# Optimization experiments

Measured on AMD Instinct MI355X. Metric: run time of the kernel, lower is better.

Reference implementation:

```python
import jax, jax.numpy as jnp
import numpy as np

N_NODES = 10000
DIM = 512
HEADS = 8
HEAD_DIM = DIM // HEADS  # 64
TOPK = 6
EPS = 1e-5
SLOPE = 0.01  # torch LeakyReLU default


def _layernorm(x, w, b):
    mu = x.mean(axis=-1, keepdims=True)
    var = ((x - mu) ** 2).mean(axis=-1, keepdims=True)
    return (x - mu) / jnp.sqrt(var + EPS) * w + b


def setup_inputs() -> dict:
    key = jax.random.key(0)
    ks = jax.random.split(key, 8)

    def w(k, shape):
        return jax.random.normal(k, shape, dtype=jnp.float32) * 0.02

    return {
        "x": jax.random.normal(ks[0], (1, N_NODES, DIM), dtype=jnp.float32),
        "fc1_w": w(ks[1], (DIM, DIM)), "fc1_b": jnp.zeros((DIM,), jnp.float32),
        "wh_w": w(ks[2], (DIM, DIM)), "wh_b": jnp.zeros((DIM,), jnp.float32),
        "wt_w": w(ks[3], (DIM, DIM)), "wt_b": jnp.zeros((DIM,), jnp.float32),
        "q_w": w(ks[4], (DIM, DIM)), "q_b": jnp.zeros((DIM,), jnp.float32),
        "kv_w": w(ks[5], (2 * DIM, DIM)), "kv_b": jnp.zeros((2 * DIM,), jnp.float32),
        "lin_w": w(ks[6], (DIM, DIM)), "lin_b": jnp.zeros((DIM,), jnp.float32),
        "norm_w": jnp.ones((DIM,), jnp.float32),
        "norm_b": jnp.zeros((DIM,), jnp.float32),
    }


def reference(x, fc1_w, fc1_b, wh_w, wh_b, wt_w, wt_b, q_w, q_b,
              kv_w, kv_b, lin_w, lin_b, norm_w, norm_b):
    # x: [1, N, DIM]
    n = x.shape[1]
    scale = HEAD_DIM ** -0.5

    x_input = x
    h = jax.nn.leaky_relu(x @ fc1_w.T + fc1_b, SLOPE)
    h = (h + h.mean(axis=1, keepdims=True)) * 0.5

    e_h = h @ wh_w.T + wh_b            # [1, N, DIM]
    e_t = h @ wt_w.T + wt_b            # [1, N, DIM]

    # dense graph-construction scores + per-row top-k neighbors
    logits = (e_h * scale) @ jnp.swapaxes(e_t, -2, -1)   # [1, N, N]
    _, topk_idx = jax.lax.top_k(logits, TOPK)            # [1, N, TOPK]

    # prototype node = most frequent tail index (torch unique+counts+argsort, top=1)
    counts = jnp.bincount(topk_idx.reshape(-1), length=n)
    top_node = jnp.argmax(counts)

    ins_top = jnp.take(x_input, top_node[None], axis=1)  # [1, 1, DIM]
    q_feat = jnp.take(h, top_node[None], axis=1)[0, 0]   # [DIM]

    # gather k=TOPK neighbor tail embeddings per node
    nb = e_t[0][topk_idx[0]]                              # [N, TOPK, DIM]

    q_heads = (q_feat @ q_w.T + q_b).reshape(HEADS, HEAD_DIM) * scale
    kv = (nb @ kv_w.T + kv_b).reshape(n, TOPK, 2, HEADS, HEAD_DIM)
    k_, v_ = kv[:, :, 0], kv[:, :, 1]                     # [N, TOPK, H, HD]

    attn = jnp.einsum('hd,nehd->nhe', q_heads, k_)        # [N, H, TOPK]
    attn = jax.nn.softmax(attn, axis=-1)
    out = jnp.einsum('nhe,nehd->nhd', attn, v_).reshape(n, DIM)

    e_nh = _layernorm(out, norm_w, norm_b)[None]          # [1, N, DIM]

    s = _layernorm(e_h + e_nh, norm_w, norm_b)
    s = jax.nn.leaky_relu(s @ lin_w.T + lin_b, SLOPE)     # dropout = identity (eval)
    embedding = s + x_input
    return embedding, ins_top
```

## Files before the change

### kernel.cpp

```cpp
#include <hip/hip_runtime.h>
#include <hip/hip_bf16.h>
#include <math.h>

#define N_NODES 10000
#define DIM 512
#define TOPK 6
#define NCHUNK 10
#define CHUNK 1024
#define NL 4
#define NCK 8
#define NC2 16
#define SLOPE 0.01
#define LN_EPS 1e-5f

typedef short bf16x8 __attribute__((ext_vector_type(8)));
typedef float f32x4 __attribute__((ext_vector_type(4)));
typedef double f64x4 __attribute__((ext_vector_type(4)));

__device__ __forceinline__ unsigned pack_key(float v, int idx)
{
    unsigned b = __float_as_uint(v);
    unsigned m = b ^ ((unsigned)((int)b >> 31) | 0x80000000u);
    return (m & 0xFFFFC000u) | (16383u - (unsigned)idx);
}

template <int D>
__device__ __forceinline__ void insert_u(unsigned (&k)[D], unsigned nk)
{
    if (nk > k[D - 1]) {
        k[D - 1] = nk;
#pragma unroll
        for (int s = D - 1; s > 0; s--) {
            unsigned hi = max(k[s], k[s - 1]);
            unsigned lo = min(k[s], k[s - 1]);
            k[s - 1] = hi; k[s] = lo;
        }
    }
}

template <int D>
__device__ __forceinline__ void insert_desc(float (&v)[D], int (&id)[D], float nv, int ni)
{
    if (nv > v[D - 1] || (nv == v[D - 1] && ni < id[D - 1])) {
        v[D - 1] = nv; id[D - 1] = ni;
#pragma unroll
        for (int s = D - 1; s > 0; s--) {
            bool sw = (v[s] > v[s - 1]) || (v[s] == v[s - 1] && id[s] < id[s - 1]);
            float tv = v[s]; int ti = id[s];
            if (sw) { v[s] = v[s - 1]; id[s] = id[s - 1]; v[s - 1] = tv; id[s - 1] = ti; }
        }
    }
}

__device__ __forceinline__ void gload16(const void* g, void* l)
{
    __builtin_amdgcn_global_load_lds(
        (const __attribute__((address_space(1))) void*)g,
        (__attribute__((address_space(3))) void*)l, 16, 0, 0);
}

__global__ __launch_bounds__(256) void colsum_part64(
    const double* __restrict__ h, double* __restrict__ part, int n, int nb)
{
    int b = blockIdx.x;
    int rows_per = (n + nb - 1) / nb;
    int r0 = b * rows_per, r1 = min(n, r0 + rows_per);
    int t = threadIdx.x;
    double s0 = 0.0, s1 = 0.0;
    for (int i = r0; i < r1; i++) {
        s0 += h[(size_t)i * DIM + t];
        s1 += h[(size_t)i * DIM + t + 256];
    }
    part[b * DIM + t] = s0;
    part[b * DIM + t + 256] = s1;
}

__global__ void colmean64(const double* __restrict__ part, double* __restrict__ mean,
                          int nb, int n)
{
    int j = blockIdx.x * blockDim.x + threadIdx.x;
    if (j < DIM) {
        double s = 0.0;
        for (int b = 0; b < nb; b++) s += part[b * DIM + j];
        mean[j] = s / (double)n;
    }
}

__global__ void hmix64(double* __restrict__ h, const double* __restrict__ mean, int total)
{
    int i = blockIdx.x * blockDim.x + threadIdx.x;
    if (i < total) h[i] = (h[i] + mean[i & (DIM - 1)]) * 0.5;
}

__global__ void cast_d2f_bf(const double* __restrict__ in, float* __restrict__ outf,
                            short* __restrict__ outb, int total)
{
    int i = blockIdx.x * blockDim.x + threadIdx.x;
    if (i < total) {
        float f = (float)in[i];
        outf[i] = f;
        __hip_bfloat16 b = __float2bfloat16(f);
        outb[i] = *reinterpret_cast<short*>(&b);
    }
}

__global__ void cast_f2b(const float* __restrict__ in, short* __restrict__ out, int total)
{
    int i = blockIdx.x * blockDim.x + threadIdx.x;
    if (i < total) {
        __hip_bfloat16 b = __float2bfloat16(in[i]);
        out[i] = *reinterpret_cast<short*>(&b);
    }
}

template <int POST, bool AF32>
__global__ __launch_bounds__(256, 4) void mfma_gemm_f64(
    const void* __restrict__ Av, const float* __restrict__ W,
    const float* __restrict__ bias, double* __restrict__ C,
    int n, int K, int M)
{
    __shared__ double As[64][18];
    __shared__ double Bs[64][18];
    const int t = threadIdx.x, lane = t & 63, wid = t >> 6;
    const int lx = lane & 15, q = lane >> 4;
    const int wr = (wid >> 1) * 32, wc = (wid & 1) * 32;
    const int i0 = blockIdx.x * 64, j0 = blockIdx.y * 64;

    f64x4 acc[2][2];
#pragma unroll
    for (int a = 0; a < 2; a++)
#pragma unroll
        for (int b = 0; b < 2; b++) acc[a][b] = (f64x4)0.0;

    const int srow = t >> 2, skq = (t & 3) * 4;
    int gi = i0 + srow; if (gi >= n) gi = n - 1;
    const int gj = j0 + srow;
    const float*  wrow = W + (size_t)gj * K + skq;
    const float*  af32 = (const float*)Av + (size_t)gi * K + skq;
    const double* af64 = (const double*)Av + (size_t)gi * K + skq;

    for (int k0 = 0; k0 < K; k0 += 16) {
        __syncthreads();
        if (AF32) {
            float4 v = *(const float4*)(af32 + k0);
            As[srow][skq]     = (double)v.x; As[srow][skq + 1] = (double)v.y;
            As[srow][skq + 2] = (double)v.z; As[srow][skq + 3] = (double)v.w;
        } else {
            double2 v0 = *(const double2*)(af64 + k0);
            double2 v1 = *(const double2*)(af64 + k0 + 2);
            As[srow][skq]     = v0.x; As[srow][skq + 1] = v0.y;
            As[srow][skq + 2] = v1.x; As[srow][skq + 3] = v1.y;
        }
        float4 wv = *(const float4*)(wrow + k0);
        Bs[srow][skq]     = (double)wv.x; Bs[srow][skq + 1] = (double)wv.y;
        Bs[srow][skq + 2] = (double)wv.z; Bs[srow][skq + 3] = (double)wv.w;
        __syncthreads();

#pragma unroll
        for (int ks = 0; ks < 4; ks++) {
            double a0 = As[wr + lx][ks * 4 + q];
            double a1 = As[wr + 16 + lx][ks * 4 + q];
            double b0 = Bs[wc + lx][ks * 4 + q];
            double b1 = Bs[wc + 16 + lx][ks * 4 + q];
            acc[0][0] = __builtin_amdgcn_mfma_f64_16x16x4f64(a0, b0, acc[0][0], 0, 0, 0);
            acc[0][1] = __builtin_amdgcn_mfma_f64_16x16x4f64(a0, b1, acc[0][1], 0, 0, 0);
            acc[1][0] = __builtin_amdgcn_mfma_f64_16x16x4f64(a1, b0, acc[1][0], 0, 0, 0);
            acc[1][1] = __builtin_amdgcn_mfma_f64_16x16x4f64(a1, b1, acc[1][1], 0, 0, 0);
        }
    }

#pragma unroll
    for (int rf = 0; rf < 2; rf++)
#pragma unroll
        for (int cf = 0; cf < 2; cf++)
#pragma unroll
            for (int reg = 0; reg < 4; reg++) {
                int gi2 = i0 + wr + rf * 16 + q * 4 + reg;
                int gj2 = j0 + wc + cf * 16 + lx;
                if (gi2 < n) {
                    double v = acc[rf][cf][reg] + (double)bias[gj2];
                    if (POST == 1) v = (v >= 0.0) ? v : v * SLOPE;
                    C[(size_t)gi2 * M + gj2] = v;
                }
            }
}

__global__ __launch_bounds__(256, 3) void logits_topk_mfma(
    const short* __restrict__ eh, const short* __restrict__ et,
    unsigned* __restrict__ pk, int n)
{
    __shared__ short As[2][4096];
    __shared__ short Bs[2][4096];
    const int t = threadIdx.x;
    const int lane = t & 63, wid = t >> 6;
    const int lx = lane & 15, q = lane >> 4;

    int id = blockIdx.x, bx, chunk;
    if (id < 632) { chunk = id & 7; bx = id >> 3; }
    else { int r = id - 632; chunk = 8 + (r & 1); bx = r >> 1; }
    const int i0 = bx * 128;
    const int wbase = wid * 32;

    const int jlo = chunk * CHUNK;
    const int jhi = min(n, jlo + CHUNK);
    const int nj = (jhi - jlo + 127) >> 7;
    const int np = nj * 16;

    const int sslot = (t & 3) ^ ((t >> 3) & 3);
    const short* aP[2];
    const short* bP[2];
#pragma unroll
    for (int is = 0; is < 2; is++) {
        int row = is * 64 + (t >> 2);
        int ra = i0 + row; if (ra >= n) ra = n - 1;
        aP[is] = eh + (size_t)ra * DIM + sslot * 8;
    }
    const int slotq = (q ^ ((lx >> 1) & 3)) * 8;
    const int aOff = (wbase + lx) * 32 + slotq;
    const int bOff = lx * 32 + slotq;

    unsigned keys[8][NL];
#pragma unroll
    for (int r = 0; r < 8; r++)
#pragma unroll
        for (int s = 0; s < NL; s++) keys[r][s] = 0u;

    f32x4 acc[2][8];
#pragma unroll
    for (int rf = 0; rf < 2; rf++)
#pragma unroll
        for (int cf = 0; cf < 8; cf++) acc[rf][cf] = (f32x4)0.f;

    auto STAGE = [&](int buf, int ph) {
        int kk = ph & 15;
        if (kk == 0) {
            int j0 = jlo + (ph >> 4) * 128;
#pragma unroll
            for (int is = 0; is < 2; is++) {
                int row = is * 64 + (t >> 2);
                int rb = j0 + row; if (rb >= n) rb = n - 1;
                bP[is] = et + (size_t)rb * DIM + sslot * 8;
            }
        }
        int ko = kk * 32;
#pragma unroll
        for (int is = 0; is < 2; is++) {
            gload16(aP[is] + ko, &As[buf][is * 2048 + wid * 512]);
            gload16(bP[is] + ko, &Bs[buf][is * 2048 + wid * 512]);
        }
    };

    STAGE(0, 0);
    for (int p = 0; p < np; ++p) {
        __builtin_amdgcn_sched_barrier(0);
        __builtin_amdgcn_s_barrier();
        __builtin_amdgcn_sched_barrier(0);
        if (p + 1 < np) {
            STAGE((p + 1) & 1, p + 1);
            asm volatile("s_waitcnt vmcnt(4)" ::: "memory");
        } else {
            asm volatile("s_waitcnt vmcnt(0)" ::: "memory");
        }
        __builtin_amdgcn_sched_barrier(0);
        __builtin_amdgcn_s_barrier();
        __builtin_amdgcn_sched_barrier(0);

        const short* Ab = As[p & 1];
        const short* Bb = Bs[p & 1];
        bf16x8 a0 = *(const bf16x8*)(Ab + aOff);
        bf16x8 a1 = *(const bf16x8*)(Ab + aOff + 512);
#pragma unroll
        for (int cf = 0; cf < 8; cf++) {
            bf16x8 bw = *(const bf16x8*)(Bb + bOff + cf * 512);
            acc[0][cf] = __builtin_amdgcn_mfma_f32_16x16x32_bf16(
                a0, bw, acc[0][cf], 0, 0, 0);
            acc[1][cf] = __builtin_amdgcn_mfma_f32_16x16x32_bf16(
                a1, bw, acc[1][cf], 0, 0, 0);
        }

        if ((p & 15) == 15) {
            int j0 = jlo + (p >> 4) * 128;
#pragma unroll
            for (int rf = 0; rf < 2; rf++)
#pragma unroll
                for (int cf = 0; cf < 8; cf++) {
                    int gj = j0 + cf * 16 + lx;
                    if (gj < n) {
#pragma unroll
                        for (int reg = 0; reg < 4; reg++)
                            insert_u<NL>(keys[rf * 4 + reg],
                                         pack_key(acc[rf][cf][reg], gj));
                    }
                    acc[rf][cf] = (f32x4)0.f;
                }
        }
    }

#pragma unroll
    for (int rr = 0; rr < 8; rr++) {
        unsigned mk[NCK];
#pragma unroll
        for (int s = 0; s < NL; s++) mk[s] = keys[rr][s];
#pragma unroll
        for (int s = NL; s < NCK; s++) mk[s] = 0u;
        for (int m = 1; m < 16; m <<= 1) {
            unsigned sv[NCK];
#pragma unroll
            for (int s = 0; s < NCK; s++) sv[s] = mk[s];
#pragma unroll
            for (int s = 0; s < NCK; s++) {
                unsigned ov = (unsigned)__shfl_xor((int)sv[s], m);
                insert_u<NCK>(mk, ov);
            }
        }
        if (lx == 0) {
            int rf = rr >> 2, reg = rr & 3;
            int grow = i0 + wbase + rf * 16 + q * 4 + reg;
            if (grow < n) {
#pragma unroll
                for (int s = 0; s < NCK; s++)
                    pk[((size_t)chunk * N_NODES + grow) * NCK + s] = mk[s];
            }
        }
    }
}

template <int POST>
__global__ __launch_bounds__(256, 3) void mfma_gemm_bf16(
    const short* __restrict__ A, const short* __restrict__ W,
    const float* __restrict__ bias, const float* __restrict__ res,
    float* __restrict__ C, int n, int M)
{
    __shared__ short As[2][8192];
    __shared__ short Bs[2][8192];
    const int t = threadIdx.x;
    const int lane = t & 63, wid = t >> 6;
    const int lx = lane & 15, q = lane >> 4;
    const int lx7 = lane & 7;
    const int i0 = blockIdx.x * 128;
    const int j0 = blockIdx.y * 128;
    const int wbase = wid * 32;
    const int srl = lane >> 3;
    const int swz = (lane & 7) ^ srl;

    const short* aP[4];
    const short* bP[4];
#pragma unroll
    for (int is = 0; is < 4; is++) {
        int ra = i0 + is * 32 + wid * 8 + srl; if (ra >= n) ra = n - 1;
        aP[is] = A + (size_t)ra * DIM + swz * 8;
        int rb = j0 + is * 32 + wid * 8 + srl;
        bP[is] = W + (size_t)rb * DIM + swz * 8;
    }
    int aIdx[2], bIdx[2];
#pragma unroll
    for (int ks = 0; ks < 2; ks++) {
        int kap = (ks * 4 + q) ^ lx7;
        aIdx[ks] = (wbase + lx) * 64 + kap * 8;
        bIdx[ks] = lx * 64 + kap * 8;
    }

    f32x4 acc[2][8];
#pragma unroll
    for (int rf = 0; rf < 2; rf++)
#pragma unroll
        for (int cf = 0; cf < 8; cf++) acc[rf][cf] = (f32x4)0.f;

    auto STAGE = [&](int buf, int kk) {
        int ko = kk * 64;
        short* ab = &As[buf][wid * 512];
        short* bb = &Bs[buf][wid * 512];
#pragma unroll
        for (int is = 0; is < 4; is++) {
            gload16(aP[is] + ko, ab + is * 2048);
            gload16(bP[is] + ko, bb + is * 2048);
        }
    };

    STAGE(0, 0);
    for (int p = 0; p < 8; ++p) {
        __builtin_amdgcn_sched_barrier(0);
        __builtin_amdgcn_s_barrier();
        __builtin_amdgcn_sched_barrier(0);
        if (p + 1 < 8) {
            STAGE((p + 1) & 1, p + 1);
            asm volatile("s_waitcnt vmcnt(8)" ::: "memory");
        } else {
            asm volatile("s_waitcnt vmcnt(0)" ::: "memory");
        }
        __builtin_amdgcn_sched_barrier(0);
        __builtin_amdgcn_s_barrier();
        __builtin_amdgcn_sched_barrier(0);

        const short* Ab = As[p & 1];
        const short* Bb = Bs[p & 1];
#pragma unroll
        for (int ks = 0; ks < 2; ks++) {
            bf16x8 a0 = *(const bf16x8*)(Ab + aIdx[ks]);
            bf16x8 a1 = *(const bf16x8*)(Ab + aIdx[ks] + 1024);
#pragma unroll
            for (int cf = 0; cf < 8; cf++) {
                bf16x8 bw = *(const bf16x8*)(Bb + bIdx[ks] + cf * 1024);
                acc[0][cf] = __builtin_amdgcn_mfma_f32_16x16x32_bf16(
                    a0, bw, acc[0][cf], 0, 0, 0);
                acc[1][cf] = __builtin_amdgcn_mfma_f32_16x16x32_bf16(
                    a1, bw, acc[1][cf], 0, 0, 0);
            }
        }
    }

#pragma unroll
    for (int rf = 0; rf < 2; rf++)
#pragma unroll
        for (int cf = 0; cf < 8; cf++)
#pragma unroll
            for (int reg = 0; reg < 4; reg++) {
                int gi = i0 + wbase + rf * 16 + q * 4 + reg;
                int gj = j0 + cf * 16 + lx;
                if (gi < n) {
                    float v = acc[rf][cf][reg] + bias[gj];
                    if (POST >= 1) v = (v >= 0.f) ? v : v * SLOPE;
                    if (POST == 2) v += res[(size_t)gi * M + gj];
                    C[(size_t)gi * M + gj] = v;
                }
            }
}

__global__ void merge_chunks16(const unsigned* __restrict__ pk,
                               int* __restrict__ cand, int n)
{
    int row = blockIdx.x * blockDim.x + threadIdx.x;
    if (row >= n) return;
    unsigned bk[NC2];
#pragma unroll
    for (int s = 0; s < NC2; s++) bk[s] = 0u;
    for (int c = 0; c < NCHUNK; c++) {
#pragma unroll
        for (int s = 0; s < NCK; s++)
            insert_u<NC2>(bk, pk[((size_t)c * n + row) * NCK + s]);
    }
#pragma unroll
    for (int s = 0; s < NC2; s++)
        cand[row * NC2 + s] = 16383 - (int)(bk[s] & 16383u);
}

__global__ __launch_bounds__(64) void refine16(
    const double* __restrict__ ehd, const double* __restrict__ etd,
    const int* __restrict__ cand, int* __restrict__ tki, int n)
{
    int row = blockIdx.x;
    int lane = threadIdx.x;
    int c = lane >> 2, sub = lane & 3;
    int j = cand[row * NC2 + c];
    const double* er = ehd + (size_t)row * DIM;
    const double* tr = etd + (size_t)j * DIM;
    double s = 0.0;
#pragma unroll 8
    for (int k = sub; k < DIM; k += 4) s += er[k] * tr[k];
    s += __shfl_down(s, 2);
    s += __shfl_down(s, 1);
    double mine = __shfl(s, lane & ~3);
    int rank = 0;
#pragma unroll
    for (int m = 0; m < NC2; m++) {
        double vm = __shfl(s, m * 4);
        int jm = __shfl(j, m * 4);
        bool better = (vm > mine) || (vm == mine && jm < j);
        rank += better ? 1 : 0;
    }
    if (sub == 0 && rank < TOPK) tki[row * TOPK + rank] = j;
}

__global__ void count_kernel(const int* __restrict__ tki, int* __restrict__ counts, int total)
{
    int i = blockIdx.x * blockDim.x + threadIdx.x;
    if (i < total) atomicAdd(&counts[tki[i]], 1);
}

__global__ __launch_bounds__(1024) void argmax_kernel(
    const int* __restrict__ counts, int n, const float* __restrict__ x,
    int* __restrict__ topn, float* __restrict__ out_ins)
{
    __shared__ unsigned long long red[1024];
    int t = threadIdx.x;
    unsigned long long best = 0;
    for (int j = t; j < n; j += 1024) {
        unsigned long long key =
            ((unsigned long long)(unsigned)counts[j] << 32) | (unsigned)(n - 1 - j);
        if (key > best) best = key;
    }
    red[t] = best;
    __syncthreads();
    for (int s = 512; s > 0; s >>= 1) {
        if (t < s && red[t + s] > red[t]) red[t] = red[t + s];
        __syncthreads();
    }
    int tn = n - 1 - (int)(red[0] & 0xffffffffu);
    if (t == 0) *topn = tn;
    if (t < DIM) out_ins[t] = x[(size_t)tn * DIM + t];
}

__global__ __launch_bounds__(512) void qheads_kernel(
    const double* __restrict__ h2d, const int* __restrict__ topn,
    const float* __restrict__ qw, const float* __restrict__ qb, float* __restrict__ qh)
{
    __shared__ float qf[DIM];
    int t = threadIdx.x;
    int tn = *topn;
    qf[t] = (float)h2d[(size_t)tn * DIM + t];
    __syncthreads();
    int w = t >> 6, lane = t & 63;
    int jrow = blockIdx.x * 8 + w;
    float s = 0.f;
    for (int k = lane; k < DIM; k += 64) s += qf[k] * qw[(size_t)jrow * DIM + k];
#pragma unroll
    for (int m = 32; m > 0; m >>= 1) s += __shfl_down(s, m);
    if (lane == 0) qh[jrow] = (s + qb[jrow]) * 0.125f;
}

__global__ __launch_bounds__(512) void scores_kernel(
    const float* __restrict__ E, const float* __restrict__ qh, float* __restrict__ sc)
{
    int i = blockIdx.x;
    int t = threadIdx.x, w = t >> 6, lane = t & 63;
    float v = qh[t] * E[(size_t)i * 1024 + t];
#pragma unroll
    for (int m = 32; m > 0; m >>= 1) v += __shfl_down(v, m);
    if (lane == 0) sc[i * 8 + w] = v;
}

__global__ __launch_bounds__(512) void attn_ln_kernel(
    const float* __restrict__ E, const float* __restrict__ sc,
    const int* __restrict__ tki, const float* __restrict__ eh,
    const float* __restrict__ nw, const float* __restrict__ nbias,
    short* __restrict__ sprb, int n)
{
    __shared__ int nb[TOPK];
    __shared__ float red[16];
    __shared__ float stats[2];
    const int i = blockIdx.x;
    const int t = threadIdx.x;
    const int h = t >> 6, lane = t & 63;
    if (t < TOPK) nb[t] = tki[i * TOPK + t];
    __syncthreads();

    float myse = 0.f;
    if (lane < TOPK) myse = sc[(size_t)nb[lane] * 8 + h];
    float se[TOPK];
#pragma unroll
    for (int e = 0; e < TOPK; e++) se[e] = __shfl(myse, e);
    float mx = se[0];
#pragma unroll
    for (int e = 1; e < TOPK; e++) mx = fmaxf(mx, se[e]);
    float wsum = 0.f, w[TOPK];
#pragma unroll
    for (int e = 0; e < TOPK; e++) { w[e] = expf(se[e] - mx); wsum += w[e]; }
    float inv = 1.f / wsum;

    float o = 0.f;
#pragma unroll
    for (int e = 0; e < TOPK; e++) o += w[e] * E[(size_t)nb[e] * 1024 + 512 + t];
    o *= inv;

    float s1 = o, s2 = o * o;
#pragma unroll
    for (int m = 32; m > 0; m >>= 1) { s1 += __shfl_down(s1, m); s2 += __shfl_down(s2, m); }
    if (lane == 0) { red[h] = s1; red[h + 8] = s2; }
    __syncthreads();
    if (t == 0) {
        float a = 0.f, b = 0.f;
#pragma unroll
        for (int k = 0; k < 8; k++) { a += red[k]; b += red[k + 8]; }
        float mu = a * (1.f / 512.f);
        float var = b * (1.f / 512.f) - mu * mu;
        stats[0] = mu; stats[1] = rsqrtf(var + LN_EPS);
    }
    __syncthreads();
    float enh = (o - stats[0]) * stats[1] * nw[t] + nbias[t];
    float t2 = eh[(size_t)i * DIM + t] + enh;
    __syncthreads();

    s1 = t2; s2 = t2 * t2;
#pragma unroll
    for (int m = 32; m > 0; m >>= 1) { s1 += __shfl_down(s1, m); s2 += __shfl_down(s2, m); }
    if (lane == 0) { red[h] = s1; red[h + 8] = s2; }
    __syncthreads();
    if (t == 0) {
        float a = 0.f, b = 0.f;
#pragma unroll
        for (int k = 0; k < 8; k++) { a += red[k]; b += red[k + 8]; }
        float mu = a * (1.f / 512.f);
        float var = b * (1.f / 512.f) - mu * mu;
        stats[0] = mu; stats[1] = rsqrtf(var + LN_EPS);
    }
    __syncthreads();
    float sv = (t2 - stats[0]) * stats[1] * nw[t] + nbias[t];
    __hip_bfloat16 bb = __float2bfloat16(sv);
    sprb[(size_t)i * DIM + t] = *reinterpret_cast<short*>(&bb);
}

extern "C" void kernel_launch(void* const* d_in, const int* in_sizes, int n_in,
                              void* d_out, int out_size, void* d_ws, size_t ws_size,
                              hipStream_t stream)
{
    const float* x     = (const float*)d_in[0];
    const float* fc1_w = (const float*)d_in[1];
    const float* fc1_b = (const float*)d_in[2];
    const float* wh_w  = (const float*)d_in[3];
    const float* wh_b  = (const float*)d_in[4];
    const float* wt_w  = (const float*)d_in[5];
    const float* wt_b  = (const float*)d_in[6];
    const float* q_w   = (const float*)d_in[7];
    const float* q_b   = (const float*)d_in[8];
    const float* kv_w  = (const float*)d_in[9];
    const float* kv_b  = (const float*)d_in[10];
    const float* lin_w = (const float*)d_in[11];
    const float* lin_b = (const float*)d_in[12];
    const float* nw    = (const float*)d_in[13];
    const float* nbias = (const float*)d_in[14];
    float* out = (float*)d_out;

    const int n = N_NODES;
    size_t off = 0;
    auto take = [&](size_t bytes) -> void* {
        void* p = (void*)((char*)d_ws + off);
        off += (bytes + 255) & ~(size_t)255;
        return p;
    };
    double* h2d  = (double*)take((size_t)n * DIM * 8);
    double* ehd  = (double*)take((size_t)n * DIM * 8);
    double* etd  = (double*)take((size_t)n * DIM * 8);
    float*  ehf  = (float*)take((size_t)n * DIM * 4);
    float*  etf  = (float*)take((size_t)n * DIM * 4);
    short*  ehb  = (short*)take((size_t)n * DIM * 2);
    short*  etb  = (short*)take((size_t)n * DIM * 2);
    unsigned* pk = (unsigned*)take((size_t)NCHUNK * n * NCK * 4);
    int*    cand = (int*)take((size_t)n * NC2 * 4);
    int*    tki  = (int*)take((size_t)n * TOPK * 4);
    int*    counts = (int*)take((size_t)n * 4);
    int*    topn = (int*)take(256);
    float*  qh   = (float*)take(DIM * 4);
    float*  sc   = (float*)take((size_t)n * 8 * 4);
    double* part = (double*)take((size_t)160 * DIM * 8);
    double* mean = (double*)take(DIM * 8);
    short*  kvwb = (short*)take((size_t)1024 * DIM * 2);
    short*  linwb = (short*)take((size_t)512 * DIM * 2);
    float* E    = (float*)h2d;
    short* sprb = (short*)etf;

    hipMemsetAsync(counts, 0, n * sizeof(int), stream);

    dim3 b256(256);
    const int RB64 = (n + 63) / 64;
    const int RB2  = (n + 127) / 128;

    mfma_gemm_f64<1, true><<<dim3(RB64, 8), b256, 0, stream>>>(
        x, fc1_w, fc1_b, h2d, n, DIM, DIM);
    colsum_part64<<<dim3(160), b256, 0, stream>>>(h2d, part, n, 160);
    colmean64<<<dim3(2), b256, 0, stream>>>(part, mean, 160, n);
    hmix64<<<dim3((n * DIM) / 256), b256, 0, stream>>>(h2d, mean, n * DIM);
    mfma_gemm_f64<0, false><<<dim3(RB64, 8), b256, 0, stream>>>(
        h2d, wh_w, wh_b, ehd, n, DIM, DIM);
    mfma_gemm_f64<0, false><<<dim3(RB64, 8), b256, 0, stream>>>(
        h2d, wt_w, wt_b, etd, n, DIM, DIM);
    cast_d2f_bf<<<dim3((n * DIM) / 256), b256, 0, stream>>>(ehd, ehf, ehb, n * DIM);
    cast_d2f_bf<<<dim3((n * DIM) / 256), b256, 0, stream>>>(etd, etf, etb, n * DIM);
    cast_f2b<<<dim3((1024 * DIM + 255) / 256), b256, 0, stream>>>(kv_w, kvwb, 1024 * DIM);
    cast_f2b<<<dim3((512 * DIM + 255) / 256), b256, 0, stream>>>(lin_w, linwb, 512 * DIM);

    logits_topk_mfma<<<dim3(632 + 2 * RB2), b256, 0, stream>>>(ehb, etb, pk, n);
    merge_chunks16<<<dim3((n + 255) / 256), b256, 0, stream>>>(pk, cand, n);
    refine16<<<dim3(n), dim3(64), 0, stream>>>(ehd, etd, cand, tki, n);

    count_kernel<<<dim3((n * TOPK + 255) / 256), b256, 0, stream>>>(tki, counts, n * TOPK);
    argmax_kernel<<<dim3(1), dim3(1024), 0, stream>>>(counts, n, x, topn,
                                                      out + (size_t)n * DIM);
    qheads_kernel<<<dim3(64), dim3(512), 0, stream>>>(h2d, topn, q_w, q_b, qh);
    mfma_gemm_bf16<0><<<dim3(RB2, 8), b256, 0, stream>>>(
        etb, kvwb, kv_b, nullptr, E, n, 1024);
    scores_kernel<<<dim3(n), dim3(512), 0, stream>>>(E, qh, sc);
    attn_ln_kernel<<<dim3(n), dim3(512), 0, stream>>>(E, sc, tki, ehf, nw, nbias, sprb, n);
    mfma_gemm_bf16<2><<<dim3(RB2, 4), b256, 0, stream>>>(
        sprb, linwb, lin_b, x, out, n, 512);
}
```

Baseline: 860.8 us.

## Split top-k column chunks finer, prefetch GEMM tiles, merge cast launches

The logits/top-k kernel now splits the column range into 20 half-size chunks instead of 10, doubling the grid to improve occupancy and load balance, and the merge kernel reads twice as many partial key lists. The main loop is unrolled by two with fixed buffer indices. The f64 GEMM prefetches the next K-slice into registers before the compute loop, and the separate cast kernels are fused into two launches. The trade-off is more partial-key traffic and merge work, plus extra register pressure in the GEMM.

```diff
diff --git a/kernel.cpp b/kernel.cpp
--- a/kernel.cpp
+++ b/kernel.cpp
@@ -5,8 +5,8 @@
 #define N_NODES 10000
 #define DIM 512
 #define TOPK 6
-#define NCHUNK 10
-#define CHUNK 1024
+#define NHC 20
+#define HCHUNK 512
 #define NL 4
 #define NCK 8
 #define NC2 16
@@ -34,20 +34,6 @@
             unsigned hi = max(k[s], k[s - 1]);
             unsigned lo = min(k[s], k[s - 1]);
             k[s - 1] = hi; k[s] = lo;
-        }
-    }
-}
-
-template <int D>
-__device__ __forceinline__ void insert_desc(float (&v)[D], int (&id)[D], float nv, int ni)
-{
-    if (nv > v[D - 1] || (nv == v[D - 1] && ni < id[D - 1])) {
-        v[D - 1] = nv; id[D - 1] = ni;
-#pragma unroll
-        for (int s = D - 1; s > 0; s--) {
-            bool sw = (v[s] > v[s - 1]) || (v[s] == v[s - 1] && id[s] < id[s - 1]);
-            float tv = v[s]; int ti = id[s];
-            if (sw) { v[s] = v[s - 1]; id[s] = id[s - 1]; v[s - 1] = tv; id[s - 1] = ti; }
         }
     }
 }
@@ -92,24 +78,31 @@
     if (i < total) h[i] = (h[i] + mean[i & (DIM - 1)]) * 0.5;
 }
 
-__global__ void cast_d2f_bf(const double* __restrict__ in, float* __restrict__ outf,
-                            short* __restrict__ outb, int total)
+__global__ void cast_d2f_bf2(const double* __restrict__ in1, float* __restrict__ of1,
+                             short* __restrict__ ob1, const double* __restrict__ in2,
+                             float* __restrict__ of2, short* __restrict__ ob2, int total)
 {
     int i = blockIdx.x * blockDim.x + threadIdx.x;
-    if (i < total) {
-        float f = (float)in[i];
-        outf[i] = f;
-        __hip_bfloat16 b = __float2bfloat16(f);
-        outb[i] = *reinterpret_cast<short*>(&b);
-    }
-}
-
-__global__ void cast_f2b(const float* __restrict__ in, short* __restrict__ out, int total)
+    const double* in = (i < total) ? in1 : in2;
+    float* of = (i < total) ? of1 : of2;
+    short* ob = (i < total) ? ob1 : ob2;
+    int idx = (i < total) ? i : i - total;
+    float f = (float)in[idx];
+    of[idx] = f;
+    __hip_bfloat16 b = __float2bfloat16(f);
+    ob[idx] = *reinterpret_cast<short*>(&b);
+}
+
+__global__ void cast_f2b2(const float* __restrict__ in1, short* __restrict__ o1, int n1,
+                          const float* __restrict__ in2, short* __restrict__ o2, int n2)
 {
     int i = blockIdx.x * blockDim.x + threadIdx.x;
-    if (i < total) {
-        __hip_bfloat16 b = __float2bfloat16(in[i]);
-        out[i] = *reinterpret_cast<short*>(&b);
+    const float* in = (i < n1) ? in1 : in2;
+    short* o = (i < n1) ? o1 : o2;
+    int idx = (i < n1) ? i : i - n1;
+    if (i < n1 + n2) {
+        __hip_bfloat16 b = __float2bfloat16(in[idx]);
+        o[idx] = *reinterpret_cast<short*>(&b);
     }
 }
 
@@ -139,21 +132,29 @@
     const float*  af32 = (const float*)Av + (size_t)gi * K + skq;
     const double* af64 = (const double*)Av + (size_t)gi * K + skq;
 
+    float4 wv = *(const float4*)(wrow);
+    float4 av;
+    double2 a0v, a1v;
+    if (AF32) av = *(const float4*)(af32);
+    else { a0v = *(const double2*)(af64); a1v = *(const double2*)(af64 + 2); }
+
     for (int k0 = 0; k0 < K; k0 += 16) {
         __syncthreads();
         if (AF32) {
-            float4 v = *(const float4*)(af32 + k0);
-            As[srow][skq]     = (double)v.x; As[srow][skq + 1] = (double)v.y;
-            As[srow][skq + 2] = (double)v.z; As[srow][skq + 3] = (double)v.w;
+            As[srow][skq]     = (double)av.x; As[srow][skq + 1] = (double)av.y;
+            As[srow][skq + 2] = (double)av.z; As[srow][skq + 3] = (double)av.w;
         } else {
-            double2 v0 = *(const double2*)(af64 + k0);
-            double2 v1 = *(const double2*)(af64 + k0 + 2);
-            As[srow][skq]     = v0.x; As[srow][skq + 1] = v0.y;
-            As[srow][skq + 2] = v1.x; As[srow][skq + 3] = v1.y;
-        }
-        float4 wv = *(const float4*)(wrow + k0);
+            As[srow][skq]     = a0v.x; As[srow][skq + 1] = a0v.y;
+            As[srow][skq + 2] = a1v.x; As[srow][skq + 3] = a1v.y;
+        }
         Bs[srow][skq]     = (double)wv.x; Bs[srow][skq + 1] = (double)wv.y;
         Bs[srow][skq + 2] = (double)wv.z; Bs[srow][skq + 3] = (double)wv.w;
+        if (k0 + 16 < K) {
+            wv = *(const float4*)(wrow + k0 + 16);
+            if (AF32) av = *(const float4*)(af32 + k0 + 16);
+            else { a0v = *(const double2*)(af64 + k0 + 16);
+                   a1v = *(const double2*)(af64 + k0 + 18); }
+        }
         __syncthreads();
 
 #pragma unroll
@@ -195,14 +196,14 @@
     const int lane = t & 63, wid = t >> 6;
     const int lx = lane & 15, q = lane >> 4;
 
-    int id = blockIdx.x, bx, chunk;
-    if (id < 632) { chunk = id & 7; bx = id >> 3; }
-    else { int r = id - 632; chunk = 8 + (r & 1); bx = r >> 1; }
+    int id = blockIdx.x, bx, hc;
+    if (id < 1264) { hc = id & 15; bx = id >> 4; }
+    else { int r = id - 1264; hc = 16 + (r & 3); bx = r >> 2; }
     const int i0 = bx * 128;
     const int wbase = wid * 32;
 
-    const int jlo = chunk * CHUNK;
-    const int jhi = min(n, jlo + CHUNK);
+    const int jlo = hc * HCHUNK;
+    const int jhi = min(n, jlo + HCHUNK);
     const int nj = (jhi - jlo + 127) >> 7;
     const int np = nj * 16;
 
@@ -250,13 +251,13 @@
         }
     };
 
-    STAGE(0, 0);
-    for (int p = 0; p < np; ++p) {
+    auto PHASE = [&](int p, const short* Ab, const short* Bb,
+                     short* AbN_unused, int curbuf) {
         __builtin_amdgcn_sched_barrier(0);
         __builtin_amdgcn_s_barrier();
         __builtin_amdgcn_sched_barrier(0);
         if (p + 1 < np) {
-            STAGE((p + 1) & 1, p + 1);
+            STAGE(curbuf ^ 1, p + 1);
             asm volatile("s_waitcnt vmcnt(4)" ::: "memory");
         } else {
             asm volatile("s_waitcnt vmcnt(0)" ::: "memory");
@@ -265,8 +266,6 @@
         __builtin_amdgcn_s_barrier();
         __builtin_amdgcn_sched_barrier(0);
 
-        const short* Ab = As[p & 1];
-        const short* Bb = Bs[p & 1];
         bf16x8 a0 = *(const bf16x8*)(Ab + aOff);
         bf16x8 a1 = *(const bf16x8*)(Ab + aOff + 512);
 #pragma unroll
@@ -294,6 +293,12 @@
                     acc[rf][cf] = (f32x4)0.f;
                 }
         }
+    };
+
+    STAGE(0, 0);
+    for (int p = 0; p < np; p += 2) {
+        PHASE(p,     As[0], Bs[0], nullptr, 0);
+        PHASE(p + 1, As[1], Bs[1], nullptr, 1);
     }
 
 #pragma unroll
@@ -319,7 +324,7 @@
             if (grow < n) {
 #pragma unroll
                 for (int s = 0; s < NCK; s++)
-                    pk[((size_t)chunk * N_NODES + grow) * NCK + s] = mk[s];
+                    pk[((size_t)hc * N_NODES + grow) * NCK + s] = mk[s];
             }
         }
     }
@@ -434,7 +439,7 @@
     unsigned bk[NC2];
 #pragma unroll
     for (int s = 0; s < NC2; s++) bk[s] = 0u;
-    for (int c = 0; c < NCHUNK; c++) {
+    for (int c = 0; c < NHC; c++) {
 #pragma unroll
         for (int s = 0; s < NCK; s++)
             insert_u<NC2>(bk, pk[((size_t)c * n + row) * NCK + s]);
@@ -634,7 +639,7 @@
     float*  etf  = (float*)take((size_t)n * DIM * 4);
     short*  ehb  = (short*)take((size_t)n * DIM * 2);
     short*  etb  = (short*)take((size_t)n * DIM * 2);
-    unsigned* pk = (unsigned*)take((size_t)NCHUNK * n * NCK * 4);
+    unsigned* pk = (unsigned*)take((size_t)NHC * n * NCK * 4);
     int*    cand = (int*)take((size_t)n * NC2 * 4);
     int*    tki  = (int*)take((size_t)n * TOPK * 4);
     int*    counts = (int*)take((size_t)n * 4);
@@ -663,12 +668,12 @@
         h2d, wh_w, wh_b, ehd, n, DIM, DIM);
     mfma_gemm_f64<0, false><<<dim3(RB64, 8), b256, 0, stream>>>(
         h2d, wt_w, wt_b, etd, n, DIM, DIM);
-    cast_d2f_bf<<<dim3((n * DIM) / 256), b256, 0, stream>>>(ehd, ehf, ehb, n * DIM);
-    cast_d2f_bf<<<dim3((n * DIM) / 256), b256, 0, stream>>>(etd, etf, etb, n * DIM);
-    cast_f2b<<<dim3((1024 * DIM + 255) / 256), b256, 0, stream>>>(kv_w, kvwb, 1024 * DIM);
-    cast_f2b<<<dim3((512 * DIM + 255) / 256), b256, 0, stream>>>(lin_w, linwb, 512 * DIM);
-
-    logits_topk_mfma<<<dim3(632 + 2 * RB2), b256, 0, stream>>>(ehb, etb, pk, n);
+    cast_d2f_bf2<<<dim3((2 * n * DIM) / 256), b256, 0, stream>>>(
+        ehd, ehf, ehb, etd, etf, etb, n * DIM);
+    cast_f2b2<<<dim3((1536 * DIM + 255) / 256), b256, 0, stream>>>(
+        kv_w, kvwb, 1024 * DIM, lin_w, linwb, 512 * DIM);
+
+    logits_topk_mfma<<<dim3(79 * NHC), b256, 0, stream>>>(ehb, etb, pk, n);
     merge_chunks16<<<dim3((n + 255) / 256), b256, 0, stream>>>(pk, cand, n);
     refine16<<<dim3(n), dim3(64), 0, stream>>>(ehd, etd, cand, tki, n);
 
```

New measurement: 920.7 us. +7.0%, slower.

## Fuse mean-mixing into f64 GEMMs, widen GEMM tiles, triple-buffer logits, fuse counting

Applied to the files above, without the earlier changes.

The h-mixing step now happens inside the A-tile load of the wh/wt f64 GEMMs, which removes the separate hmix pass over h. The f64 GEMM tile is widened to 64x128 with register prefetch of the next K slice. The logits/top-k kernel moves from double to triple-buffered LDS staging. The count kernel is folded into refine16 via atomics. The cast kernels are vectorized, the two weight casts are merged into one launch, and the unused fp32 copy of et is dropped. Together these cut launches and memory passes, at the cost of more LDS and register pressure, which may lower occupancy.

```diff
diff --git a/kernel.cpp b/kernel.cpp
--- a/kernel.cpp
+++ b/kernel.cpp
@@ -38,20 +38,6 @@
     }
 }
 
-template <int D>
-__device__ __forceinline__ void insert_desc(float (&v)[D], int (&id)[D], float nv, int ni)
-{
-    if (nv > v[D - 1] || (nv == v[D - 1] && ni < id[D - 1])) {
-        v[D - 1] = nv; id[D - 1] = ni;
-#pragma unroll
-        for (int s = D - 1; s > 0; s--) {
-            bool sw = (v[s] > v[s - 1]) || (v[s] == v[s - 1] && id[s] < id[s - 1]);
-            float tv = v[s]; int ti = id[s];
-            if (sw) { v[s] = v[s - 1]; id[s] = id[s - 1]; v[s - 1] = tv; id[s - 1] = ti; }
-        }
-    }
-}
-
 __device__ __forceinline__ void gload16(const void* g, void* l)
 {
     __builtin_amdgcn_global_load_lds(
@@ -86,93 +72,124 @@
     }
 }
 
-__global__ void hmix64(double* __restrict__ h, const double* __restrict__ mean, int total)
-{
-    int i = blockIdx.x * blockDim.x + threadIdx.x;
-    if (i < total) h[i] = (h[i] + mean[i & (DIM - 1)]) * 0.5;
-}
-
-__global__ void cast_d2f_bf(const double* __restrict__ in, float* __restrict__ outf,
-                            short* __restrict__ outb, int total)
-{
-    int i = blockIdx.x * blockDim.x + threadIdx.x;
-    if (i < total) {
-        float f = (float)in[i];
-        outf[i] = f;
-        __hip_bfloat16 b = __float2bfloat16(f);
-        outb[i] = *reinterpret_cast<short*>(&b);
-    }
-}
-
-__global__ void cast_f2b(const float* __restrict__ in, short* __restrict__ out, int total)
-{
-    int i = blockIdx.x * blockDim.x + threadIdx.x;
-    if (i < total) {
-        __hip_bfloat16 b = __float2bfloat16(in[i]);
-        out[i] = *reinterpret_cast<short*>(&b);
-    }
-}
-
-template <int POST, bool AF32>
+__global__ void cast_eh(const double* __restrict__ in, float* __restrict__ of,
+                        short* __restrict__ ob)
+{
+    int i = (blockIdx.x * blockDim.x + threadIdx.x) * 4;
+    double2 v0 = *(const double2*)(in + i);
+    double2 v1 = *(const double2*)(in + i + 2);
+    float4 f = make_float4((float)v0.x, (float)v0.y, (float)v1.x, (float)v1.y);
+    *(float4*)(of + i) = f;
+    __hip_bfloat16 b0 = __float2bfloat16(f.x), b1 = __float2bfloat16(f.y);
+    __hip_bfloat16 b2 = __float2bfloat16(f.z), b3 = __float2bfloat16(f.w);
+    short4 s = make_short4(*(short*)&b0, *(short*)&b1, *(short*)&b2, *(short*)&b3);
+    *(short4*)(ob + i) = s;
+}
+
+__global__ void cast_et(const double* __restrict__ in, short* __restrict__ ob)
+{
+    int i = (blockIdx.x * blockDim.x + threadIdx.x) * 4;
+    double2 v0 = *(const double2*)(in + i);
+    double2 v1 = *(const double2*)(in + i + 2);
+    __hip_bfloat16 b0 = __float2bfloat16((float)v0.x), b1 = __float2bfloat16((float)v0.y);
+    __hip_bfloat16 b2 = __float2bfloat16((float)v1.x), b3 = __float2bfloat16((float)v1.y);
+    short4 s = make_short4(*(short*)&b0, *(short*)&b1, *(short*)&b2, *(short*)&b3);
+    *(short4*)(ob + i) = s;
+}
+
+__global__ void cast_wb(const float* __restrict__ in1, short* __restrict__ o1, int n1,
+                        const float* __restrict__ in2, short* __restrict__ o2)
+{
+    int i = (blockIdx.x * blockDim.x + threadIdx.x) * 4;
+    const float* in = (i < n1) ? in1 + i : in2 + (i - n1);
+    short* o = (i < n1) ? o1 + i : o2 + (i - n1);
+    float4 f = *(const float4*)in;
+    __hip_bfloat16 b0 = __float2bfloat16(f.x), b1 = __float2bfloat16(f.y);
+    __hip_bfloat16 b2 = __float2bfloat16(f.z), b3 = __float2bfloat16(f.w);
+    *(short4*)o = make_short4(*(short*)&b0, *(short*)&b1, *(short*)&b2, *(short*)&b3);
+}
+
+template <int POST, bool AF32, bool MIX>
 __global__ __launch_bounds__(256, 4) void mfma_gemm_f64(
     const void* __restrict__ Av, const float* __restrict__ W,
-    const float* __restrict__ bias, double* __restrict__ C,
-    int n, int K, int M)
+    const float* __restrict__ bias, const double* __restrict__ mn,
+    double* __restrict__ C, int n, int K, int M)
 {
     __shared__ double As[64][18];
-    __shared__ double Bs[64][18];
+    __shared__ double Bs[128][18];
     const int t = threadIdx.x, lane = t & 63, wid = t >> 6;
     const int lx = lane & 15, q = lane >> 4;
-    const int wr = (wid >> 1) * 32, wc = (wid & 1) * 32;
-    const int i0 = blockIdx.x * 64, j0 = blockIdx.y * 64;
-
-    f64x4 acc[2][2];
+    const int wr = (wid >> 1) * 32, wc = (wid & 1) * 64;
+    const int i0 = blockIdx.x * 64, j0 = blockIdx.y * 128;
+
+    f64x4 acc[2][4];
 #pragma unroll
     for (int a = 0; a < 2; a++)
 #pragma unroll
-        for (int b = 0; b < 2; b++) acc[a][b] = (f64x4)0.0;
-
-    const int srow = t >> 2, skq = (t & 3) * 4;
-    int gi = i0 + srow; if (gi >= n) gi = n - 1;
-    const int gj = j0 + srow;
-    const float*  wrow = W + (size_t)gj * K + skq;
-    const float*  af32 = (const float*)Av + (size_t)gi * K + skq;
-    const double* af64 = (const double*)Av + (size_t)gi * K + skq;
+        for (int b = 0; b < 4; b++) acc[a][b] = (f64x4)0.0;
+
+    const int arow = t >> 2, askq = (t & 3) * 4;
+    int gi = i0 + arow; if (gi >= n) gi = n - 1;
+    const float*  af32 = (const float*)Av + (size_t)gi * K + askq;
+    const double* af64 = (const double*)Av + (size_t)gi * K + askq;
+    const int brow = t >> 1, bskq = (t & 1) * 8;
+    const float* wrow = W + (size_t)(j0 + brow) * K + bskq;
+
+    float4 wv0 = *(const float4*)(wrow);
+    float4 wv1 = *(const float4*)(wrow + 4);
+    float4 av;
+    double2 a0v, a1v;
+    if (AF32) av = *(const float4*)(af32);
+    else { a0v = *(const double2*)(af64); a1v = *(const double2*)(af64 + 2); }
 
     for (int k0 = 0; k0 < K; k0 += 16) {
         __syncthreads();
+        double m0 = 0, m1 = 0, m2 = 0, m3 = 0;
+        if (MIX) {
+            double2 mv0 = *(const double2*)(mn + k0 + askq);
+            double2 mv1 = *(const double2*)(mn + k0 + askq + 2);
+            m0 = mv0.x; m1 = mv0.y; m2 = mv1.x; m3 = mv1.y;
+        }
         if (AF32) {
-            float4 v = *(const float4*)(af32 + k0);
-            As[srow][skq]     = (double)v.x; As[srow][skq + 1] = (double)v.y;
-            As[srow][skq + 2] = (double)v.z; As[srow][skq + 3] = (double)v.w;
+            As[arow][askq]     = (double)av.x; As[arow][askq + 1] = (double)av.y;
+            As[arow][askq + 2] = (double)av.z; As[arow][askq + 3] = (double)av.w;
+        } else if (MIX) {
+            As[arow][askq]     = (a0v.x + m0) * 0.5; As[arow][askq + 1] = (a0v.y + m1) * 0.5;
+            As[arow][askq + 2] = (a1v.x + m2) * 0.5; As[arow][askq + 3] = (a1v.y + m3) * 0.5;
         } else {
-            double2 v0 = *(const double2*)(af64 + k0);
-            double2 v1 = *(const double2*)(af64 + k0 + 2);
-            As[srow][skq]     = v0.x; As[srow][skq + 1] = v0.y;
-            As[srow][skq + 2] = v1.x; As[srow][skq + 3] = v1.y;
-        }
-        float4 wv = *(const float4*)(wrow + k0);
-        Bs[srow][skq]     = (double)wv.x; Bs[srow][skq + 1] = (double)wv.y;
-        Bs[srow][skq + 2] = (double)wv.z; Bs[srow][skq + 3] = (double)wv.w;
+            As[arow][askq]     = a0v.x; As[arow][askq + 1] = a0v.y;
+            As[arow][askq + 2] = a1v.x; As[arow][askq + 3] = a1v.y;
+        }
+        Bs[brow][bskq]     = (double)wv0.x; Bs[brow][bskq + 1] = (double)wv0.y;
+        Bs[brow][bskq + 2] = (double)wv0.z; Bs[brow][bskq + 3] = (double)wv0.w;
+        Bs[brow][bskq + 4] = (double)wv1.x; Bs[brow][bskq + 5] = (double)wv1.y;
+        Bs[brow][bskq + 6] = (double)wv1.z; Bs[brow][bskq + 7] = (double)wv1.w;
+        if (k0 + 16 < K) {
+            wv0 = *(const float4*)(wrow + k0 + 16);
+            wv1 = *(const float4*)(wrow + k0 + 20);
+            if (AF32) av = *(const float4*)(af32 + k0 + 16);
+            else { a0v = *(const double2*)(af64 + k0 + 16);
+                   a1v = *(const double2*)(af64 + k0 + 18); }
+        }
         __syncthreads();
 
 #pragma unroll
         for (int ks = 0; ks < 4; ks++) {
             double a0 = As[wr + lx][ks * 4 + q];
             double a1 = As[wr + 16 + lx][ks * 4 + q];
-            double b0 = Bs[wc + lx][ks * 4 + q];
-            double b1 = Bs[wc + 16 + lx][ks * 4 + q];
-            acc[0][0] = __builtin_amdgcn_mfma_f64_16x16x4f64(a0, b0, acc[0][0], 0, 0, 0);
-            acc[0][1] = __builtin_amdgcn_mfma_f64_16x16x4f64(a0, b1, acc[0][1], 0, 0, 0);
-            acc[1][0] = __builtin_amdgcn_mfma_f64_16x16x4f64(a1, b0, acc[1][0], 0, 0, 0);
-            acc[1][1] = __builtin_amdgcn_mfma_f64_16x16x4f64(a1, b1, acc[1][1], 0, 0, 0);
+#pragma unroll
+            for (int cf = 0; cf < 4; cf++) {
+                double b = Bs[wc + cf * 16 + lx][ks * 4 + q];
+                acc[0][cf] = __builtin_amdgcn_mfma_f64_16x16x4f64(a0, b, acc[0][cf], 0, 0, 0);
+                acc[1][cf] = __builtin_amdgcn_mfma_f64_16x16x4f64(a1, b, acc[1][cf], 0, 0, 0);
+            }
         }
     }
 
 #pragma unroll
     for (int rf = 0; rf < 2; rf++)
 #pragma unroll
-        for (int cf = 0; cf < 2; cf++)
+        for (int cf = 0; cf < 4; cf++)
 #pragma unroll
             for (int reg = 0; reg < 4; reg++) {
                 int gi2 = i0 + wr + rf * 16 + q * 4 + reg;
@@ -189,8 +206,8 @@
     const short* __restrict__ eh, const short* __restrict__ et,
     unsigned* __restrict__ pk, int n)
 {
-    __shared__ short As[2][4096];
-    __shared__ short Bs[2][4096];
+    __shared__ short As[3 * 4096];
+    __shared__ short Bs[3 * 4096];
     const int t = threadIdx.x;
     const int lane = t & 63, wid = t >> 6;
     const int lx = lane & 15, q = lane >> 4;
@@ -245,18 +262,23 @@
         int ko = kk * 32;
 #pragma unroll
         for (int is = 0; is < 2; is++) {
-            gload16(aP[is] + ko, &As[buf][is * 2048 + wid * 512]);
-            gload16(bP[is] + ko, &Bs[buf][is * 2048 + wid * 512]);
+            gload16(aP[is] + ko, &As[buf * 4096 + is * 2048 + wid * 512]);
+            gload16(bP[is] + ko, &Bs[buf * 4096 + is * 2048 + wid * 512]);
         }
     };
 
     STAGE(0, 0);
+    STAGE(1, 1);
+    int cb = 0;
     for (int p = 0; p < np; ++p) {
         __builtin_amdgcn_sched_barrier(0);
         __builtin_amdgcn_s_barrier();
         __builtin_amdgcn_sched_barrier(0);
-        if (p + 1 < np) {
-            STAGE((p + 1) & 1, p + 1);
+        if (p + 2 < np) {
+            int nb = cb + 2; if (nb >= 3) nb -= 3;
+            STAGE(nb, p + 2);
+            asm volatile("s_waitcnt vmcnt(8)" ::: "memory");
+        } else if (p + 1 < np) {
             asm volatile("s_waitcnt vmcnt(4)" ::: "memory");
         } else {
             asm volatile("s_waitcnt vmcnt(0)" ::: "memory");
@@ -265,8 +287,8 @@
         __builtin_amdgcn_s_barrier();
         __builtin_amdgcn_sched_barrier(0);
 
-        const short* Ab = As[p & 1];
-        const short* Bb = Bs[p & 1];
+        const short* Ab = As + cb * 4096;
+        const short* Bb = Bs + cb * 4096;
         bf16x8 a0 = *(const bf16x8*)(Ab + aOff);
         bf16x8 a1 = *(const bf16x8*)(Ab + aOff + 512);
 #pragma unroll
@@ -294,6 +316,7 @@
                     acc[rf][cf] = (f32x4)0.f;
                 }
         }
+        cb = (cb == 2) ? 0 : cb + 1;
     }
 
 #pragma unroll
@@ -446,7 +469,8 @@
 
 __global__ __launch_bounds__(64) void refine16(
     const double* __restrict__ ehd, const double* __restrict__ etd,
-    const int* __restrict__ cand, int* __restrict__ tki, int n)
+    const int* __restrict__ cand, int* __restrict__ tki,
+    int* __restrict__ counts, int n)
 {
     int row = blockIdx.x;
     int lane = threadIdx.x;
@@ -468,13 +492,10 @@
         bool better = (vm > mine) || (vm == mine && jm < j);
         rank += better ? 1 : 0;
     }
-    if (sub == 0 && rank < TOPK) tki[row * TOPK + rank] = j;
-}
-
-__global__ void count_kernel(const int* __restrict__ tki, int* __restrict__ counts, int total)
-{
-    int i = blockIdx.x * blockDim.x + threadIdx.x;
-    if (i < total) atomicAdd(&counts[tki[i]], 1);
+    if (sub == 0 && rank < TOPK) {
+        tki[row * TOPK + rank] = j;
+        atomicAdd(&counts[j], 1);
+    }
 }
 
 __global__ __launch_bounds__(1024) void argmax_kernel(
@@ -501,13 +522,14 @@
 }
 
 __global__ __launch_bounds__(512) void qheads_kernel(
-    const double* __restrict__ h2d, const int* __restrict__ topn,
-    const float* __restrict__ qw, const float* __restrict__ qb, float* __restrict__ qh)
+    const double* __restrict__ h2d, const double* __restrict__ mn,
+    const int* __restrict__ topn, const float* __restrict__ qw,
+    const float* __restrict__ qb, float* __restrict__ qh)
 {
     __shared__ float qf[DIM];
     int t = threadIdx.x;
     int tn = *topn;
-    qf[t] = (float)h2d[(size_t)tn * DIM + t];
+    qf[t] = (float)((h2d[(size_t)tn * DIM + t] + mn[t]) * 0.5);
     __syncthreads();
     int w = t >> 6, lane = t & 63;
     int jrow = blockIdx.x * 8 + w;
@@ -631,9 +653,9 @@
     double* ehd  = (double*)take((size_t)n * DIM * 8);
     double* etd  = (double*)take((size_t)n * DIM * 8);
     float*  ehf  = (float*)take((size_t)n * DIM * 4);
-    float*  etf  = (float*)take((size_t)n * DIM * 4);
     short*  ehb  = (short*)take((size_t)n * DIM * 2);
     short*  etb  = (short*)take((size_t)n * DIM * 2);
+    short*  sprb = (short*)take((size_t)n * DIM * 2);
     unsigned* pk = (unsigned*)take((size_t)NCHUNK * n * NCK * 4);
     int*    cand = (int*)take((size_t)n * NC2 * 4);
     int*    tki  = (int*)take((size_t)n * TOPK * 4);
@@ -645,8 +667,7 @@
     double* mean = (double*)take(DIM * 8);
     short*  kvwb = (short*)take((size_t)1024 * DIM * 2);
     short*  linwb = (short*)take((size_t)512 * DIM * 2);
-    float* E    = (float*)h2d;
-    short* sprb = (short*)etf;
+    float* E = (float*)h2d;
 
     hipMemsetAsync(counts, 0, n * sizeof(int), stream);
 
@@ -654,28 +675,26 @@
     const int RB64 = (n + 63) / 64;
     const int RB2  = (n + 127) / 128;
 
-    mfma_gemm_f64<1, true><<<dim3(RB64, 8), b256, 0, stream>>>(
-        x, fc1_w, fc1_b, h2d, n, DIM, DIM);
+    mfma_gemm_f64<1, true, false><<<dim3(RB64, 4), b256, 0, stream>>>(
+        x, fc1_w, fc1_b, nullptr, h2d, n, DIM, DIM);
     colsum_part64<<<dim3(160), b256, 0, stream>>>(h2d, part, n, 160);
     colmean64<<<dim3(2), b256, 0, stream>>>(part, mean, 160, n);
-    hmix64<<<dim3((n * DIM) / 256), b256, 0, stream>>>(h2d, mean, n * DIM);
-    mfma_gemm_f64<0, false><<<dim3(RB64, 8), b256, 0, stream>>>(
-        h2d, wh_w, wh_b, ehd, n, DIM, DIM);
-    mfma_gemm_f64<0, false><<<dim3(RB64, 8), b256, 0, stream>>>(
-        h2d, wt_w, wt_b, etd, n, DIM, DIM);
-    cast_d2f_bf<<<dim3((n * DIM) / 256), b256, 0, stream>>>(ehd, ehf, ehb, n * DIM);
-    cast_d2f_bf<<<dim3((n * DIM) / 256), b256, 0, stream>>>(etd, etf, etb, n * DIM);
-    cast_f2b<<<dim3((1024 * DIM + 255) / 256), b256, 0, stream>>>(kv_w, kvwb, 1024 * DIM);
-    cast_f2b<<<dim3((512 * DIM + 255) / 256), b256, 0, stream>>>(lin_w, linwb, 512 * DIM);
+    mfma_gemm_f64<0, false, true><<<dim3(RB64, 4), b256, 0, stream>>>(
+        h2d, wh_w, wh_b, mean, ehd, n, DIM, DIM);
+    mfma_gemm_f64<0, false, true><<<dim3(RB64, 4), b256, 0, stream>>>(
+        h2d, wt_w, wt_b, mean, etd, n, DIM, DIM);
+    cast_eh<<<dim3((n * DIM) / 1024), b256, 0, stream>>>(ehd, ehf, ehb);
+    cast_et<<<dim3((n * DIM) / 1024), b256, 0, stream>>>(etd, etb);
+    cast_wb<<<dim3((1536 * DIM) / 1024), b256, 0, stream>>>(
+        kv_w, kvwb, 1024 * DIM, lin_w, linwb);
 
     logits_topk_mfma<<<dim3(632 + 2 * RB2), b256, 0, stream>>>(ehb, etb, pk, n);
     merge_chunks16<<<dim3((n + 255) / 256), b256, 0, stream>>>(pk, cand, n);
-    refine16<<<dim3(n), dim3(64), 0, stream>>>(ehd, etd, cand, tki, n);
-
-    count_kernel<<<dim3((n * TOPK + 255) / 256), b256, 0, stream>>>(tki, counts, n * TOPK);
+    refine16<<<dim3(n), dim3(64), 0, stream>>>(ehd, etd, cand, tki, counts, n);
+
     argmax_kernel<<<dim3(1), dim3(1024), 0, stream>>>(counts, n, x, topn,
                                                       out + (size_t)n * DIM);
-    qheads_kernel<<<dim3(64), dim3(512), 0, stream>>>(h2d, topn, q_w, q_b, qh);
+    qheads_kernel<<<dim3(64), dim3(512), 0, stream>>>(h2d, mean, topn, q_w, q_b, qh);
     mfma_gemm_bf16<0><<<dim3(RB2, 8), b256, 0, stream>>>(
         etb, kvwb, kv_b, nullptr, E, n, 1024);
     scores_kernel<<<dim3(n), dim3(512), 0, stream>>>(E, qh, sc);
```

After: 920.3 us. +6.9%, slower.
